# Optimization experiments

Measured on AMD Instinct MI355X. Metric: run time of the kernel, lower is better.

The kernel has to match this reference:

```python
import jax, jax.numpy as jnp
import numpy as np

B, C_IN, C_QKV, N = 8, 12, 36, 4096

def setup_inputs() -> dict:
    key = jax.random.key(0)
    ks = jax.random.split(key, 9)
    s_in = 1.0 / np.sqrt(C_IN)
    s_o = 1.0 / np.sqrt(C_QKV)
    return {
        "x": jax.random.normal(ks[0], (B, C_IN, N), dtype=jnp.float32),
        "wq": jax.random.uniform(ks[1], (C_QKV, C_IN), jnp.float32, -s_in, s_in),
        "bq": jax.random.uniform(ks[2], (C_QKV,), jnp.float32, -s_in, s_in),
        "wk": jax.random.uniform(ks[3], (C_QKV, C_IN), jnp.float32, -s_in, s_in),
        "bk": jax.random.uniform(ks[4], (C_QKV,), jnp.float32, -s_in, s_in),
        "wv": jax.random.uniform(ks[5], (C_QKV, C_IN), jnp.float32, -s_in, s_in),
        "bv": jax.random.uniform(ks[6], (C_QKV,), jnp.float32, -s_in, s_in),
        "wo": jax.random.uniform(ks[7], (C_IN, C_QKV), jnp.float32, -s_o, s_o),
        "bo": jax.random.uniform(ks[8], (C_IN,), jnp.float32, -s_o, s_o),
    }

def _conv1x1(w, b, x):
    # 1x1 Conv1d == channel-mixing matmul: [o,i] @ [b,i,n] -> [b,o,n]
    return jnp.einsum('oi,bin->bon', w, x) + b[None, :, None]

def reference(x, wq, bq, wk, bk, wv, bv, wo, bo):
    scale = 1.0 / jnp.sqrt(jnp.float32(x.shape[1]))  # 1/sqrt(12)
    q = _conv1x1(wq, bq, x)  # [B, 36, N]
    k = _conv1x1(wk, bk, x)
    v = _conv1x1(wv, bv, x)
    # inter = k^T @ q : scores[b,n,m] = sum_c k[b,c,n] * q[b,c,m]
    scores = jnp.einsum('bcn,bcm->bnm', k, q) * scale  # [B, N, N]
    weights = jax.nn.softmax(scores, axis=-1)
    attn = jnp.einsum('bcn,bnm->bcm', v, weights)  # v @ weights, [B, 36, N]
    return _conv1x1(wo, bo, attn)  # [B, 12, N]
```

## Files before the change

### kernel.cpp

```cpp
#include <hip/hip_runtime.h>
#include <hip/hip_bf16.h>
#include <math.h>

#define B 8
#define CIN 12
#define CQ 36
#define CP 48
#define N 4096
#define SCALE 0.28867513459481287f
#define LOG2E 1.4426950408889634f
#define ZSPLIT 8
#define NCHUNK (N / ZSPLIT)
#define NT (NCHUNK / 32)
#define MSPLIT 2

typedef __attribute__((ext_vector_type(4)))  short bf4_t;
typedef __attribute__((ext_vector_type(8)))  short bf8_t;
typedef __attribute__((ext_vector_type(16))) float f32x16;
typedef __attribute__((ext_vector_type(4)))  float f32x4;

__device__ __forceinline__ unsigned short f2bf(float x) {
  unsigned int u = __float_as_uint(x);
  u += 0x7FFFu + ((u >> 16) & 1u);
  return (unsigned short)(u >> 16);
}

#if __has_builtin(__builtin_amdgcn_cvt_pk_bf16_f32)
typedef __attribute__((ext_vector_type(2))) __bf16 bf16x2_t;
__device__ __forceinline__ unsigned pk2bf(float a, float b) {
  bf16x2_t v = __builtin_amdgcn_cvt_pk_bf16_f32(a, b);
  return __builtin_bit_cast(unsigned, v);
}
#else
__device__ __forceinline__ unsigned pk2bf(float a, float b) {
  return (__float_as_uint(a) >> 16) | (__float_as_uint(b) & 0xFFFF0000u);
}
#endif

__device__ __forceinline__ float bf2f(unsigned short u) {
  return __uint_as_float((unsigned)u << 16);
}

__device__ __forceinline__ float exp2fast(float x) {
#if __has_builtin(__builtin_amdgcn_exp2f)
  return __builtin_amdgcn_exp2f(x);
#else
  return exp2f(x);
#endif
}

__device__ __forceinline__ f32x4 mfma16(bf4_t a, bf4_t b, f32x4 c) {
#if __has_builtin(__builtin_amdgcn_mfma_f32_16x16x16bf16_1k)
  return __builtin_amdgcn_mfma_f32_16x16x16bf16_1k(a, b, c, 0, 0, 0);
#else
  bf8_t a8 = {a[0], a[1], a[2], a[3], 0, 0, 0, 0};
  bf8_t b8 = {b[0], b[1], b[2], b[3], 0, 0, 0, 0};
  return __builtin_amdgcn_mfma_f32_16x16x32_bf16(a8, b8, c, 0, 0, 0);
#endif
}

__device__ __forceinline__ bf8_t lds_bf8(const unsigned short* p) {
  uint2 a = *(const uint2*)p;
  uint2 b = *(const uint2*)(p + 4);
  uint4 r{a.x, a.y, b.x, b.y};
  return __builtin_bit_cast(bf8_t, r);
}
__device__ __forceinline__ void wlds16(unsigned short* p, uint4 v) {
  *(uint2*)p = uint2{v.x, v.y};
  *(uint2*)(p + 4) = uint2{v.z, v.w};
}

__global__ __launch_bounds__(256) void qkv_kernel(
    const float* __restrict__ x,
    const float* __restrict__ wq, const float* __restrict__ bq,
    const float* __restrict__ wk, const float* __restrict__ bk,
    const float* __restrict__ wv, const float* __restrict__ bv,
    unsigned short* __restrict__ qT, unsigned short* __restrict__ kT,
    unsigned short* __restrict__ vbf) {
  __shared__ float sw[CQ * CIN];
  __shared__ float sb[CQ];
  int z = blockIdx.y;
  const float* w  = (z == 0) ? wq : (z == 1) ? wk : wv;
  const float* bb = (z == 0) ? bq : (z == 1) ? bk : bv;
  float scale = (z == 1) ? SCALE * LOG2E : 1.0f;
  int tid = threadIdx.x;
  for (int e = tid; e < CQ * CIN; e += 256) sw[e] = w[e] * scale;
  if (tid < CQ) sb[tid] = bb[tid] * scale;
  __syncthreads();
  int gid = blockIdx.x * 256 + tid;
  int b = gid >> 12;
  int n = gid & (N - 1);
  float xv[CIN];
#pragma unroll
  for (int i = 0; i < CIN; ++i) xv[i] = x[(b * CIN + i) * N + n];
  if (z == 2) {
#pragma unroll
    for (int o = 0; o < CQ; ++o) {
      float a = sb[o];
#pragma unroll
      for (int i = 0; i < CIN; ++i) a += sw[o * CIN + i] * xv[i];
      vbf[((size_t)b * CP + o) * N + n] = f2bf(a);
    }
  } else {
    __attribute__((aligned(16))) unsigned row[CP / 2];
#pragma unroll
    for (int o = 0; o < CQ; o += 2) {
      float a0 = sb[o], a1 = sb[o + 1];
#pragma unroll
      for (int i = 0; i < CIN; ++i) {
        float xi = xv[i];
        a0 += sw[o * CIN + i] * xi;
        a1 += sw[(o + 1) * CIN + i] * xi;
      }
      row[o / 2] = (unsigned)f2bf(a0) | ((unsigned)f2bf(a1) << 16);
    }
    row[18] = (z == 0) ? 0x3F803F80u : 0u;
#pragma unroll
    for (int o = 19; o < CP / 2; ++o) row[o] = 0;
    unsigned short* dst = ((z == 0) ? qT : kT) + ((size_t)b * N + n) * CP;
#pragma unroll
    for (int i = 0; i < 6; ++i) *(uint4*)(dst + 8 * i) = *(const uint4*)&row[4 * i];
  }
}

__global__ __launch_bounds__(256) void stats_kernel(
    const unsigned short* __restrict__ qT, const unsigned short* __restrict__ kT,
    float* __restrict__ psum) {
  __shared__ float red[4][64];
  int tid = threadIdx.x, lane = tid & 63, wave = tid >> 6;
  int b = blockIdx.y, nblk = blockIdx.x, ms = blockIdx.z;
  int l31 = lane & 31, h = lane >> 5;
  int n0 = nblk * 64;
  size_t bN = (size_t)b * N;
  const unsigned short* krow0 = kT + (bN + n0 + l31) * CP + h * 8;
  const unsigned short* krow1 = krow0 + (size_t)32 * CP;
  bf8_t a0 = *(const bf8_t*)(krow0);
  bf8_t a1 = *(const bf8_t*)(krow0 + 16);
  bf8_t a2 = *(const bf8_t*)(krow0 + 32);
  bf8_t a3 = *(const bf8_t*)(krow1);
  bf8_t a4 = *(const bf8_t*)(krow1 + 16);
  bf8_t a5 = *(const bf8_t*)(krow1 + 32);
  float rs0[16], rs1[16];
#pragma unroll
  for (int r = 0; r < 16; ++r) { rs0[r] = 0.f; rs1[r] = 0.f; }
  const int MW = N / MSPLIT / 4;
  const unsigned short* qbase =
      qT + (bN + ms * (N / MSPLIT) + wave * MW + l31) * CP + h * 8;
#pragma unroll 2
  for (int t = 0; t < MW / 32; ++t) {
    const unsigned short* qrow2 = qbase + (size_t)t * 32 * CP;
    bf8_t b0 = *(const bf8_t*)(qrow2);
    bf8_t b1 = *(const bf8_t*)(qrow2 + 16);
    bf8_t b2 = *(const bf8_t*)(qrow2 + 32);
    f32x16 S0, S1;
#pragma unroll
    for (int r = 0; r < 16; ++r) { S0[r] = 0.f; S1[r] = 0.f; }
    S0 = __builtin_amdgcn_mfma_f32_32x32x16_bf16(a0, b0, S0, 0, 0, 0);
    S0 = __builtin_amdgcn_mfma_f32_32x32x16_bf16(a1, b1, S0, 0, 0, 0);
    S0 = __builtin_amdgcn_mfma_f32_32x32x16_bf16(a2, b2, S0, 0, 0, 0);
    S1 = __builtin_amdgcn_mfma_f32_32x32x16_bf16(a3, b0, S1, 0, 0, 0);
    S1 = __builtin_amdgcn_mfma_f32_32x32x16_bf16(a4, b1, S1, 0, 0, 0);
    S1 = __builtin_amdgcn_mfma_f32_32x32x16_bf16(a5, b2, S1, 0, 0, 0);
#pragma unroll
    for (int r = 0; r < 16; ++r) {
      rs0[r] += exp2fast(S0[r]);
      rs1[r] += exp2fast(S1[r]);
    }
  }
#pragma unroll
  for (int off = 16; off >= 1; off >>= 1)
#pragma unroll
    for (int r = 0; r < 16; ++r) {
      rs0[r] += __shfl_xor(rs0[r], off, 32);
      rs1[r] += __shfl_xor(rs1[r], off, 32);
    }
  if (l31 == 0) {
#pragma unroll
    for (int r = 0; r < 16; ++r) {
      int row = (r & 3) + 8 * (r >> 2) + 4 * h;
      red[wave][row] = rs0[r];
      red[wave][32 + row] = rs1[r];
    }
  }
  __syncthreads();
  if (tid < 64) {
    float s = red[0][tid] + red[1][tid] + red[2][tid] + red[3][tid];
    psum[((size_t)ms * B + b) * N + n0 + tid] = s;
  }
}

__global__ __launch_bounds__(256) void prep_kernel(
    const float* __restrict__ psum, unsigned short* __restrict__ kT,
    float* __restrict__ out, const float* __restrict__ bo) {
  int bx = blockIdx.x, tid = threadIdx.x;
  if (bx < B * N / 256) {
    int gid = bx * 256 + tid;
    float L = 0.f;
#pragma unroll
    for (int ms = 0; ms < MSPLIT; ++ms) L += psum[(size_t)ms * B * N + gid];
    float t = -__log2f(L);
    unsigned short hi = f2bf(t);
    unsigned short lo = f2bf(t - bf2f(hi));
    size_t base = (size_t)gid * CP;
    kT[base + 36] = hi;
    kT[base + 37] = lo;
  } else {
    int gid = (bx - B * N / 256) * 256 + tid;
    int e4 = gid * 4;
    int i = (e4 >> 12) % CIN;
    float bv = bo[i];
    *(float4*)(out + e4) = float4{bv, bv, bv, bv};
  }
}

__global__ __launch_bounds__(256, 3) void attn_kernel(
    const unsigned short* __restrict__ qT, const unsigned short* __restrict__ kT,
    const unsigned short* __restrict__ vbf, const float* __restrict__ wo,
    float* __restrict__ out) {
  __shared__ unsigned short kbuf[2][32 * 52];
  __shared__ unsigned short vbuf[2][48 * 36];
  __shared__ unsigned short plds[4][2][32 * 40];
  int tid = threadIdx.x, lane = tid & 63, wave = tid >> 6;
  int b = blockIdx.y, z = blockIdx.z, mblk = blockIdx.x;
  int l31 = lane & 31, h = lane >> 5, l15 = lane & 15, q4 = lane >> 4;
  int m0 = mblk * 256 + wave * 64;
  size_t bN = (size_t)b * N;
  bool isK0 = tid < 192;
  int r0row = isK0 ? (tid / 6) : ((tid - 192) >> 2);
  int r0c   = isK0 ? (tid % 6) : ((tid - 192) & 3);
  const unsigned short* s0 = isK0
      ? kT + (bN + z * NCHUNK + r0row) * CP + r0c * 8
      : vbf + ((size_t)b * CP + r0row) * N + z * NCHUNK + r0c * 8;
  int s0stride = isK0 ? 32 * CP : 32;
  unsigned short* dst0 = isK0 ? &kbuf[0][r0row * 52 + r0c * 8]
                              : &vbuf[0][r0row * 36 + r0c * 8];
  int dbs0 = isK0 ? 32 * 52 : 48 * 36;
  bool has1 = tid < 128;
  int r1row = (tid >> 2) + 16;
  int r1c = tid & 3;
  const unsigned short* s1 =
      vbf + ((size_t)b * CP + r1row) * N + z * NCHUNK + r1c * 8;
  unsigned short* dst1 = &vbuf[0][r1row * 36 + r1c * 8];
  const int dbs1 = 48 * 36;
  bf8_t qb[2][3];
#pragma unroll
  for (int mt = 0; mt < 2; ++mt) {
    const unsigned short* qrow = qT + (bN + m0 + mt * 32 + l31) * CP + h * 8;
    qb[mt][0] = *(const bf8_t*)(qrow);
    qb[mt][1] = *(const bf8_t*)(qrow + 16);
    qb[mt][2] = *(const bf8_t*)(qrow + 32);
  }
  bf4_t woa[3];
#pragma unroll
  for (int ct = 0; ct < 3; ++ct) {
    float4 w4 = {0.f, 0.f, 0.f, 0.f};
    int col = 16 * ct + q4 * 4;
    if (l15 < CIN && col < CQ) w4 = *(const float4*)(wo + l15 * CQ + col);
    woa[ct] = bf4_t{(short)f2bf(w4.x), (short)f2bf(w4.y),
                    (short)f2bf(w4.z), (short)f2bf(w4.w)};
  }
  f32x4 acc[2][3][2];
#pragma unroll
  for (int mt = 0; mt < 2; ++mt)
#pragma unroll
    for (int ct = 0; ct < 3; ++ct)
#pragma unroll
      for (int hm = 0; hm < 2; ++hm)
#pragma unroll
        for (int r = 0; r < 4; ++r) acc[mt][ct][hm][r] = 0.f;
  uint4 r0 = *(const uint4*)s0; s0 += s0stride;
  uint4 r1{0, 0, 0, 0};
  if (has1) { r1 = *(const uint4*)s1; s1 += 32; }
  wlds16(dst0, r0);
  if (has1) wlds16(dst1, r1);
  __syncthreads();
  for (int t = 0; t < NT; ++t) {
    int buf = t & 1;
    if (t + 1 < NT) {
      r0 = *(const uint4*)s0; s0 += s0stride;
      if (has1) { r1 = *(const uint4*)s1; s1 += 32; }
    }
    const unsigned short* kb = kbuf[buf];
    const unsigned short* vb = vbuf[buf];
    bf8_t a0 = lds_bf8(kb + l31 * 52 + h * 8);
    bf8_t a1 = lds_bf8(kb + l31 * 52 + h * 8 + 16);
    bf8_t a2 = lds_bf8(kb + l31 * 52 + h * 8 + 32);
#pragma unroll
    for (int mt = 0; mt < 2; ++mt) {
      f32x16 S;
#pragma unroll
      for (int r = 0; r < 16; ++r) S[r] = 0.f;
      S = __builtin_amdgcn_mfma_f32_32x32x16_bf16(a0, qb[mt][0], S, 0, 0, 0);
      S = __builtin_amdgcn_mfma_f32_32x32x16_bf16(a1, qb[mt][1], S, 0, 0, 0);
      S = __builtin_amdgcn_mfma_f32_32x32x16_bf16(a2, qb[mt][2], S, 0, 0, 0);
      unsigned short* pl = plds[wave][mt];
#pragma unroll
      for (int qd = 0; qd < 4; ++qd) {
        uint2 pk;
        pk.x = pk2bf(exp2fast(S[4 * qd + 0]), exp2fast(S[4 * qd + 1]));
        pk.y = pk2bf(exp2fast(S[4 * qd + 2]), exp2fast(S[4 * qd + 3]));
        *(uint2*)&pl[l31 * 40 + 8 * qd + 4 * h] = pk;
      }
    }
    bf8_t v0 = lds_bf8(vb + (0 * 16 + l15) * 36 + q4 * 8);
    bf8_t v1 = lds_bf8(vb + (1 * 16 + l15) * 36 + q4 * 8);
    bf8_t v2 = lds_bf8(vb + (2 * 16 + l15) * 36 + q4 * 8);
#pragma unroll
    for (int mt = 0; mt < 2; ++mt) {
      const unsigned short* pl = plds[wave][mt];
      bf8_t pb0 = *(const bf8_t*)&pl[l15 * 40 + q4 * 8];
      bf8_t pb1 = *(const bf8_t*)&pl[(16 + l15) * 40 + q4 * 8];
      acc[mt][0][0] = __builtin_amdgcn_mfma_f32_16x16x32_bf16(v0, pb0, acc[mt][0][0], 0, 0, 0);
      acc[mt][0][1] = __builtin_amdgcn_mfma_f32_16x16x32_bf16(v0, pb1, acc[mt][0][1], 0, 0, 0);
      acc[mt][1][0] = __builtin_amdgcn_mfma_f32_16x16x32_bf16(v1, pb0, acc[mt][1][0], 0, 0, 0);
      acc[mt][1][1] = __builtin_amdgcn_mfma_f32_16x16x32_bf16(v1, pb1, acc[mt][1][1], 0, 0, 0);
      acc[mt][2][0] = __builtin_amdgcn_mfma_f32_16x16x32_bf16(v2, pb0, acc[mt][2][0], 0, 0, 0);
      acc[mt][2][1] = __builtin_amdgcn_mfma_f32_16x16x32_bf16(v2, pb1, acc[mt][2][1], 0, 0, 0);
    }
    if (t + 1 < NT) {
      int nb = buf ^ 1;
      wlds16(dst0 + nb * dbs0, r0);
      if (has1) wlds16(dst1 + nb * dbs1, r1);
    }
    __syncthreads();
  }
#pragma unroll
  for (int mt = 0; mt < 2; ++mt)
#pragma unroll
    for (int hm = 0; hm < 2; ++hm) {
      f32x4 po = {0.f, 0.f, 0.f, 0.f};
#pragma unroll
      for (int ct = 0; ct < 3; ++ct) {
        union { uint2 u; bf4_t v; } pb;
        pb.u.x = pk2bf(acc[mt][ct][hm][0], acc[mt][ct][hm][1]);
        pb.u.y = pk2bf(acc[mt][ct][hm][2], acc[mt][ct][hm][3]);
        po = mfma16(woa[ct], pb.v, po);
      }
      if (q4 < 3) {
        float* ob = out + ((size_t)b * CIN + q4 * 4) * N + m0 + mt * 32 + hm * 16 + l15;
#pragma unroll
        for (int r = 0; r < 4; ++r) atomicAdd(ob + (size_t)r * N, po[r]);
      }
    }
}

extern "C" void kernel_launch(void* const* d_in, const int* in_sizes, int n_in,
                              void* d_out, int out_size, void* d_ws, size_t ws_size,
                              hipStream_t stream) {
  const float* x  = (const float*)d_in[0];
  const float* wq = (const float*)d_in[1];
  const float* bq = (const float*)d_in[2];
  const float* wk = (const float*)d_in[3];
  const float* bk = (const float*)d_in[4];
  const float* wv = (const float*)d_in[5];
  const float* bv = (const float*)d_in[6];
  const float* wo = (const float*)d_in[7];
  const float* bo = (const float*)d_in[8];
  float* out = (float*)d_out;

  char* ws = (char*)d_ws;
  unsigned short* qT  = (unsigned short*)ws;
  unsigned short* kT  = (unsigned short*)(ws + 3145728);
  unsigned short* vbf = (unsigned short*)(ws + 2 * 3145728);
  float* psum = (float*)(ws + 3 * 3145728);

  qkv_kernel<<<dim3(B * N / 256, 3), 256, 0, stream>>>(x, wq, bq, wk, bk, wv, bv,
                                                       qT, kT, vbf);
  stats_kernel<<<dim3(N / 64, B, MSPLIT), 256, 0, stream>>>(qT, kT, psum);
  prep_kernel<<<B * N / 256 + B * CIN * N / 1024, 256, 0, stream>>>(psum, kT, out, bo);
  attn_kernel<<<dim3(N / 256, B, ZSPLIT), 256, 0, stream>>>(qT, kT, vbf, wo, out);
}
```

Baseline: 135.9 us.

## Fuse four pipeline kernels into one cooperative mega-kernel with grid syncs

Merges the qkv, stats, prep and attention kernels into a single cooperative launch of 1024 blocks, separated by grid-wide barriers, to remove kernel-launch gaps and tail effects between the stages. The qkv stage is also reorganized so that 8 threads share each position and each computes a slice of Q, K or V. In the attention loop the P write/read is interleaved per m-tile, and the LDS buffers are shared through one raw shared array. The change risks grid.sync overhead, and the mega-kernel uses max-size register and LDS limits across all phases, which may lower occupancy. If the cooperative launch fails, it falls back to four per-phase launches.

Result: slower. 515.5 us (+279.4%).

```diff
diff --git a/kernel.cpp b/kernel.cpp
--- a/kernel.cpp
+++ b/kernel.cpp
@@ -1,6 +1,9 @@
 #include <hip/hip_runtime.h>
 #include <hip/hip_bf16.h>
+#include <hip/hip_cooperative_groups.h>
 #include <math.h>
+
+namespace cg = cooperative_groups;
 
 #define B 8
 #define CIN 12
@@ -70,278 +73,293 @@
   *(uint2*)(p + 4) = uint2{v.z, v.w};
 }
 
-__global__ __launch_bounds__(256) void qkv_kernel(
+__global__ __launch_bounds__(256, 4) void mega_kernel(
     const float* __restrict__ x,
     const float* __restrict__ wq, const float* __restrict__ bq,
     const float* __restrict__ wk, const float* __restrict__ bk,
     const float* __restrict__ wv, const float* __restrict__ bv,
+    const float* __restrict__ wo, const float* __restrict__ bo,
     unsigned short* __restrict__ qT, unsigned short* __restrict__ kT,
-    unsigned short* __restrict__ vbf) {
-  __shared__ float sw[CQ * CIN];
-  __shared__ float sb[CQ];
-  int z = blockIdx.y;
-  const float* w  = (z == 0) ? wq : (z == 1) ? wk : wv;
-  const float* bb = (z == 0) ? bq : (z == 1) ? bk : bv;
-  float scale = (z == 1) ? SCALE * LOG2E : 1.0f;
+    unsigned short* __restrict__ vbf, float* __restrict__ psum,
+    float* __restrict__ out, int phase) {
+  __shared__ __align__(16) char smraw[34048];
+  cg::grid_group grid = cg::this_grid();
   int tid = threadIdx.x;
-  for (int e = tid; e < CQ * CIN; e += 256) sw[e] = w[e] * scale;
-  if (tid < CQ) sb[tid] = bb[tid] * scale;
-  __syncthreads();
-  int gid = blockIdx.x * 256 + tid;
-  int b = gid >> 12;
-  int n = gid & (N - 1);
-  float xv[CIN];
-#pragma unroll
-  for (int i = 0; i < CIN; ++i) xv[i] = x[(b * CIN + i) * N + n];
-  if (z == 2) {
-#pragma unroll
-    for (int o = 0; o < CQ; ++o) {
-      float a = sb[o];
-#pragma unroll
-      for (int i = 0; i < CIN; ++i) a += sw[o * CIN + i] * xv[i];
-      vbf[((size_t)b * CP + o) * N + n] = f2bf(a);
-    }
-  } else {
-    __attribute__((aligned(16))) unsigned row[CP / 2];
-#pragma unroll
-    for (int o = 0; o < CQ; o += 2) {
-      float a0 = sb[o], a1 = sb[o + 1];
-#pragma unroll
-      for (int i = 0; i < CIN; ++i) {
-        float xi = xv[i];
-        a0 += sw[o * CIN + i] * xi;
-        a1 += sw[(o + 1) * CIN + i] * xi;
-      }
-      row[o / 2] = (unsigned)f2bf(a0) | ((unsigned)f2bf(a1) << 16);
-    }
-    row[18] = (z == 0) ? 0x3F803F80u : 0u;
-#pragma unroll
-    for (int o = 19; o < CP / 2; ++o) row[o] = 0;
-    unsigned short* dst = ((z == 0) ? qT : kT) + ((size_t)b * N + n) * CP;
-#pragma unroll
-    for (int i = 0; i < 6; ++i) *(uint4*)(dst + 8 * i) = *(const uint4*)&row[4 * i];
-  }
-}
-
-__global__ __launch_bounds__(256) void stats_kernel(
-    const unsigned short* __restrict__ qT, const unsigned short* __restrict__ kT,
-    float* __restrict__ psum) {
-  __shared__ float red[4][64];
-  int tid = threadIdx.x, lane = tid & 63, wave = tid >> 6;
-  int b = blockIdx.y, nblk = blockIdx.x, ms = blockIdx.z;
-  int l31 = lane & 31, h = lane >> 5;
-  int n0 = nblk * 64;
-  size_t bN = (size_t)b * N;
-  const unsigned short* krow0 = kT + (bN + n0 + l31) * CP + h * 8;
-  const unsigned short* krow1 = krow0 + (size_t)32 * CP;
-  bf8_t a0 = *(const bf8_t*)(krow0);
-  bf8_t a1 = *(const bf8_t*)(krow0 + 16);
-  bf8_t a2 = *(const bf8_t*)(krow0 + 32);
-  bf8_t a3 = *(const bf8_t*)(krow1);
-  bf8_t a4 = *(const bf8_t*)(krow1 + 16);
-  bf8_t a5 = *(const bf8_t*)(krow1 + 32);
-  float rs0[16], rs1[16];
-#pragma unroll
-  for (int r = 0; r < 16; ++r) { rs0[r] = 0.f; rs1[r] = 0.f; }
-  const int MW = N / MSPLIT / 4;
-  const unsigned short* qbase =
-      qT + (bN + ms * (N / MSPLIT) + wave * MW + l31) * CP + h * 8;
+  int bx = blockIdx.x;
+
+  if (phase == -1 || phase == 0) {
+    float* sw = (float*)smraw;
+    for (int e = tid; e < CQ * CIN; e += 256) {
+      sw[e] = wq[e];
+      sw[432 + e] = wk[e] * (SCALE * LOG2E);
+      sw[864 + e] = wv[e];
+    }
+    if (tid < CQ) {
+      sw[1296 + tid] = bq[tid];
+      sw[1332 + tid] = bk[tid] * (SCALE * LOG2E);
+      sw[1368 + tid] = bv[tid];
+    }
+    __syncthreads();
+    int p = bx * 32 + (tid >> 3);
+    int slot = tid & 7;
+    int b = p >> 12, n = p & (N - 1);
+    float xv[CIN];
+#pragma unroll
+    for (int i = 0; i < CIN; ++i) xv[i] = x[(b * CIN + i) * N + n];
+    if (slot < 6) {
+      int isK = slot >= 3 ? 1 : 0;
+      int s = slot - 3 * isK;
+      const float* w = sw + 432 * isK;
+      const float* bb2 = sw + 1296 + 36 * isK;
+      unsigned rowu[8];
+#pragma unroll
+      for (int jj = 0; jj < 8; ++jj) {
+        float a2[2];
+#pragma unroll
+        for (int e = 0; e < 2; ++e) {
+          int o = 16 * s + 2 * jj + e;
+          float a;
+          if (o < CQ) {
+            a = bb2[o];
+#pragma unroll
+            for (int i = 0; i < CIN; ++i) a += w[o * CIN + i] * xv[i];
+          } else if (o < 38 && !isK) {
+            a = 1.0f;
+          } else {
+            a = 0.f;
+          }
+          a2[e] = a;
+        }
+        rowu[jj] = pk2bf(a2[0], a2[1]);
+      }
+      unsigned short* dst = (isK ? kT : qT) + ((size_t)b * N + n) * CP + 16 * s;
+      uint4 u0{rowu[0], rowu[1], rowu[2], rowu[3]};
+      uint4 u1{rowu[4], rowu[5], rowu[6], rowu[7]};
+      *(uint4*)dst = u0;
+      *(uint4*)(dst + 8) = u1;
+    } else {
+      int s = slot - 6;
+#pragma unroll
+      for (int j = 0; j < 18; ++j) {
+        int o = 18 * s + j;
+        float a = sw[1368 + o];
+#pragma unroll
+        for (int i = 0; i < CIN; ++i) a += sw[864 + o * CIN + i] * xv[i];
+        vbf[((size_t)b * CP + o) * N + n] = f2bf(a);
+      }
+    }
+  }
+  if (phase == -1) grid.sync();
+
+  if (phase == -1 || phase == 1) {
+    float (*red)[64] = (float(*)[64])smraw;
+    int lane = tid & 63, wave = tid >> 6;
+    int nblk = bx & 63, b = (bx >> 6) & 7, ms = bx >> 9;
+    int l31 = lane & 31, h = lane >> 5;
+    int n0 = nblk * 64;
+    size_t bN = (size_t)b * N;
+    const unsigned short* krow0 = kT + (bN + n0 + l31) * CP + h * 8;
+    const unsigned short* krow1 = krow0 + (size_t)32 * CP;
+    bf8_t a0 = *(const bf8_t*)(krow0);
+    bf8_t a1 = *(const bf8_t*)(krow0 + 16);
+    bf8_t a2 = *(const bf8_t*)(krow0 + 32);
+    bf8_t a3 = *(const bf8_t*)(krow1);
+    bf8_t a4 = *(const bf8_t*)(krow1 + 16);
+    bf8_t a5 = *(const bf8_t*)(krow1 + 32);
+    float rs0[16], rs1[16];
+#pragma unroll
+    for (int r = 0; r < 16; ++r) { rs0[r] = 0.f; rs1[r] = 0.f; }
+    const int MW = N / MSPLIT / 4;
+    const unsigned short* qbase =
+        qT + (bN + ms * (N / MSPLIT) + wave * MW + l31) * CP + h * 8;
 #pragma unroll 2
-  for (int t = 0; t < MW / 32; ++t) {
-    const unsigned short* qrow2 = qbase + (size_t)t * 32 * CP;
-    bf8_t b0 = *(const bf8_t*)(qrow2);
-    bf8_t b1 = *(const bf8_t*)(qrow2 + 16);
-    bf8_t b2 = *(const bf8_t*)(qrow2 + 32);
-    f32x16 S0, S1;
-#pragma unroll
-    for (int r = 0; r < 16; ++r) { S0[r] = 0.f; S1[r] = 0.f; }
-    S0 = __builtin_amdgcn_mfma_f32_32x32x16_bf16(a0, b0, S0, 0, 0, 0);
-    S0 = __builtin_amdgcn_mfma_f32_32x32x16_bf16(a1, b1, S0, 0, 0, 0);
-    S0 = __builtin_amdgcn_mfma_f32_32x32x16_bf16(a2, b2, S0, 0, 0, 0);
-    S1 = __builtin_amdgcn_mfma_f32_32x32x16_bf16(a3, b0, S1, 0, 0, 0);
-    S1 = __builtin_amdgcn_mfma_f32_32x32x16_bf16(a4, b1, S1, 0, 0, 0);
-    S1 = __builtin_amdgcn_mfma_f32_32x32x16_bf16(a5, b2, S1, 0, 0, 0);
-#pragma unroll
-    for (int r = 0; r < 16; ++r) {
-      rs0[r] += exp2fast(S0[r]);
-      rs1[r] += exp2fast(S1[r]);
-    }
-  }
-#pragma unroll
-  for (int off = 16; off >= 1; off >>= 1)
-#pragma unroll
-    for (int r = 0; r < 16; ++r) {
-      rs0[r] += __shfl_xor(rs0[r], off, 32);
-      rs1[r] += __shfl_xor(rs1[r], off, 32);
-    }
-  if (l31 == 0) {
-#pragma unroll
-    for (int r = 0; r < 16; ++r) {
-      int row = (r & 3) + 8 * (r >> 2) + 4 * h;
-      red[wave][row] = rs0[r];
-      red[wave][32 + row] = rs1[r];
-    }
-  }
-  __syncthreads();
-  if (tid < 64) {
-    float s = red[0][tid] + red[1][tid] + red[2][tid] + red[3][tid];
-    psum[((size_t)ms * B + b) * N + n0 + tid] = s;
-  }
-}
-
-__global__ __launch_bounds__(256) void prep_kernel(
-    const float* __restrict__ psum, unsigned short* __restrict__ kT,
-    float* __restrict__ out, const float* __restrict__ bo) {
-  int bx = blockIdx.x, tid = threadIdx.x;
-  if (bx < B * N / 256) {
-    int gid = bx * 256 + tid;
-    float L = 0.f;
-#pragma unroll
-    for (int ms = 0; ms < MSPLIT; ++ms) L += psum[(size_t)ms * B * N + gid];
-    float t = -__log2f(L);
-    unsigned short hi = f2bf(t);
-    unsigned short lo = f2bf(t - bf2f(hi));
-    size_t base = (size_t)gid * CP;
-    kT[base + 36] = hi;
-    kT[base + 37] = lo;
-  } else {
-    int gid = (bx - B * N / 256) * 256 + tid;
-    int e4 = gid * 4;
-    int i = (e4 >> 12) % CIN;
-    float bv = bo[i];
-    *(float4*)(out + e4) = float4{bv, bv, bv, bv};
-  }
-}
-
-__global__ __launch_bounds__(256, 3) void attn_kernel(
-    const unsigned short* __restrict__ qT, const unsigned short* __restrict__ kT,
-    const unsigned short* __restrict__ vbf, const float* __restrict__ wo,
-    float* __restrict__ out) {
-  __shared__ unsigned short kbuf[2][32 * 52];
-  __shared__ unsigned short vbuf[2][48 * 36];
-  __shared__ unsigned short plds[4][2][32 * 40];
-  int tid = threadIdx.x, lane = tid & 63, wave = tid >> 6;
-  int b = blockIdx.y, z = blockIdx.z, mblk = blockIdx.x;
-  int l31 = lane & 31, h = lane >> 5, l15 = lane & 15, q4 = lane >> 4;
-  int m0 = mblk * 256 + wave * 64;
-  size_t bN = (size_t)b * N;
-  bool isK0 = tid < 192;
-  int r0row = isK0 ? (tid / 6) : ((tid - 192) >> 2);
-  int r0c   = isK0 ? (tid % 6) : ((tid - 192) & 3);
-  const unsigned short* s0 = isK0
-      ? kT + (bN + z * NCHUNK + r0row) * CP + r0c * 8
-      : vbf + ((size_t)b * CP + r0row) * N + z * NCHUNK + r0c * 8;
-  int s0stride = isK0 ? 32 * CP : 32;
-  unsigned short* dst0 = isK0 ? &kbuf[0][r0row * 52 + r0c * 8]
-                              : &vbuf[0][r0row * 36 + r0c * 8];
-  int dbs0 = isK0 ? 32 * 52 : 48 * 36;
-  bool has1 = tid < 128;
-  int r1row = (tid >> 2) + 16;
-  int r1c = tid & 3;
-  const unsigned short* s1 =
-      vbf + ((size_t)b * CP + r1row) * N + z * NCHUNK + r1c * 8;
-  unsigned short* dst1 = &vbuf[0][r1row * 36 + r1c * 8];
-  const int dbs1 = 48 * 36;
-  bf8_t qb[2][3];
-#pragma unroll
-  for (int mt = 0; mt < 2; ++mt) {
-    const unsigned short* qrow = qT + (bN + m0 + mt * 32 + l31) * CP + h * 8;
-    qb[mt][0] = *(const bf8_t*)(qrow);
-    qb[mt][1] = *(const bf8_t*)(qrow + 16);
-    qb[mt][2] = *(const bf8_t*)(qrow + 32);
-  }
-  bf4_t woa[3];
-#pragma unroll
-  for (int ct = 0; ct < 3; ++ct) {
-    float4 w4 = {0.f, 0.f, 0.f, 0.f};
-    int col = 16 * ct + q4 * 4;
-    if (l15 < CIN && col < CQ) w4 = *(const float4*)(wo + l15 * CQ + col);
-    woa[ct] = bf4_t{(short)f2bf(w4.x), (short)f2bf(w4.y),
-                    (short)f2bf(w4.z), (short)f2bf(w4.w)};
-  }
-  f32x4 acc[2][3][2];
-#pragma unroll
-  for (int mt = 0; mt < 2; ++mt)
-#pragma unroll
-    for (int ct = 0; ct < 3; ++ct)
-#pragma unroll
-      for (int hm = 0; hm < 2; ++hm)
-#pragma unroll
-        for (int r = 0; r < 4; ++r) acc[mt][ct][hm][r] = 0.f;
-  uint4 r0 = *(const uint4*)s0; s0 += s0stride;
-  uint4 r1{0, 0, 0, 0};
-  if (has1) { r1 = *(const uint4*)s1; s1 += 32; }
-  wlds16(dst0, r0);
-  if (has1) wlds16(dst1, r1);
-  __syncthreads();
-  for (int t = 0; t < NT; ++t) {
-    int buf = t & 1;
-    if (t + 1 < NT) {
-      r0 = *(const uint4*)s0; s0 += s0stride;
-      if (has1) { r1 = *(const uint4*)s1; s1 += 32; }
-    }
-    const unsigned short* kb = kbuf[buf];
-    const unsigned short* vb = vbuf[buf];
-    bf8_t a0 = lds_bf8(kb + l31 * 52 + h * 8);
-    bf8_t a1 = lds_bf8(kb + l31 * 52 + h * 8 + 16);
-    bf8_t a2 = lds_bf8(kb + l31 * 52 + h * 8 + 32);
+    for (int t = 0; t < MW / 32; ++t) {
+      const unsigned short* qrow2 = qbase + (size_t)t * 32 * CP;
+      bf8_t b0 = *(const bf8_t*)(qrow2);
+      bf8_t b1 = *(const bf8_t*)(qrow2 + 16);
+      bf8_t b2 = *(const bf8_t*)(qrow2 + 32);
+      f32x16 S0, S1;
+#pragma unroll
+      for (int r = 0; r < 16; ++r) { S0[r] = 0.f; S1[r] = 0.f; }
+      S0 = __builtin_amdgcn_mfma_f32_32x32x16_bf16(a0, b0, S0, 0, 0, 0);
+      S0 = __builtin_amdgcn_mfma_f32_32x32x16_bf16(a1, b1, S0, 0, 0, 0);
+      S0 = __builtin_amdgcn_mfma_f32_32x32x16_bf16(a2, b2, S0, 0, 0, 0);
+      S1 = __builtin_amdgcn_mfma_f32_32x32x16_bf16(a3, b0, S1, 0, 0, 0);
+      S1 = __builtin_amdgcn_mfma_f32_32x32x16_bf16(a4, b1, S1, 0, 0, 0);
+      S1 = __builtin_amdgcn_mfma_f32_32x32x16_bf16(a5, b2, S1, 0, 0, 0);
+#pragma unroll
+      for (int r = 0; r < 16; ++r) {
+        rs0[r] += exp2fast(S0[r]);
+        rs1[r] += exp2fast(S1[r]);
+      }
+    }
+#pragma unroll
+    for (int off = 16; off >= 1; off >>= 1)
+#pragma unroll
+      for (int r = 0; r < 16; ++r) {
+        rs0[r] += __shfl_xor(rs0[r], off, 32);
+        rs1[r] += __shfl_xor(rs1[r], off, 32);
+      }
+    if (l31 == 0) {
+#pragma unroll
+      for (int r = 0; r < 16; ++r) {
+        int row = (r & 3) + 8 * (r >> 2) + 4 * h;
+        red[wave][row] = rs0[r];
+        red[wave][32 + row] = rs1[r];
+      }
+    }
+    __syncthreads();
+    if (tid < 64) {
+      float s = red[0][tid] + red[1][tid] + red[2][tid] + red[3][tid];
+      psum[((size_t)ms * B + b) * N + n0 + tid] = s;
+    }
+  }
+  if (phase == -1) grid.sync();
+
+  if (phase == -1 || phase == 2) {
+    if (bx < 128) {
+      int gid = bx * 256 + tid;
+      float L = psum[gid] + psum[(size_t)B * N + gid];
+      float t = -__log2f(L);
+      unsigned short hi = f2bf(t);
+      unsigned short lo = f2bf(t - bf2f(hi));
+      size_t base = (size_t)gid * CP;
+      kT[base + 36] = hi;
+      kT[base + 37] = lo;
+    } else if (bx < 512) {
+      int gid = (bx - 128) * 256 + tid;
+      int e4 = gid * 4;
+      int i = (e4 >> 12) % CIN;
+      float bv2 = bo[i];
+      *(float4*)(out + e4) = float4{bv2, bv2, bv2, bv2};
+    }
+  }
+  if (phase == -1) grid.sync();
+
+  if (phase == -1 || phase == 3) {
+    unsigned short* kbuf = (unsigned short*)smraw;
+    unsigned short* vbuf = kbuf + 2 * 32 * 52;
+    unsigned short* plds = vbuf + 2 * 48 * 36;
+    int lane = tid & 63, wave = tid >> 6;
+    int mblk = bx & 15, b = (bx >> 4) & 7, z = bx >> 7;
+    int l31 = lane & 31, h = lane >> 5, l15 = lane & 15, q4 = lane >> 4;
+    int m0 = mblk * 256 + wave * 64;
+    size_t bN = (size_t)b * N;
+    bool isK0 = tid < 192;
+    int r0row = isK0 ? (tid / 6) : ((tid - 192) >> 2);
+    int r0c   = isK0 ? (tid % 6) : ((tid - 192) & 3);
+    const unsigned short* s0 = isK0
+        ? kT + (bN + z * NCHUNK + r0row) * CP + r0c * 8
+        : vbf + ((size_t)b * CP + r0row) * N + z * NCHUNK + r0c * 8;
+    int s0stride = isK0 ? 32 * CP : 32;
+    unsigned short* dst0 = isK0 ? &kbuf[r0row * 52 + r0c * 8]
+                                : &vbuf[r0row * 36 + r0c * 8];
+    int dbs0 = isK0 ? 32 * 52 : 48 * 36;
+    bool has1 = tid < 128;
+    int r1row = (tid >> 2) + 16;
+    int r1c = tid & 3;
+    const unsigned short* s1 =
+        vbf + ((size_t)b * CP + r1row) * N + z * NCHUNK + r1c * 8;
+    unsigned short* dst1 = &vbuf[r1row * 36 + r1c * 8];
+    const int dbs1 = 48 * 36;
+    bf8_t qb[2][3];
 #pragma unroll
     for (int mt = 0; mt < 2; ++mt) {
-      f32x16 S;
-#pragma unroll
-      for (int r = 0; r < 16; ++r) S[r] = 0.f;
-      S = __builtin_amdgcn_mfma_f32_32x32x16_bf16(a0, qb[mt][0], S, 0, 0, 0);
-      S = __builtin_amdgcn_mfma_f32_32x32x16_bf16(a1, qb[mt][1], S, 0, 0, 0);
-      S = __builtin_amdgcn_mfma_f32_32x32x16_bf16(a2, qb[mt][2], S, 0, 0, 0);
-      unsigned short* pl = plds[wave][mt];
-#pragma unroll
-      for (int qd = 0; qd < 4; ++qd) {
-        uint2 pk;
-        pk.x = pk2bf(exp2fast(S[4 * qd + 0]), exp2fast(S[4 * qd + 1]));
-        pk.y = pk2bf(exp2fast(S[4 * qd + 2]), exp2fast(S[4 * qd + 3]));
-        *(uint2*)&pl[l31 * 40 + 8 * qd + 4 * h] = pk;
-      }
-    }
-    bf8_t v0 = lds_bf8(vb + (0 * 16 + l15) * 36 + q4 * 8);
-    bf8_t v1 = lds_bf8(vb + (1 * 16 + l15) * 36 + q4 * 8);
-    bf8_t v2 = lds_bf8(vb + (2 * 16 + l15) * 36 + q4 * 8);
-#pragma unroll
-    for (int mt = 0; mt < 2; ++mt) {
-      const unsigned short* pl = plds[wave][mt];
-      bf8_t pb0 = *(const bf8_t*)&pl[l15 * 40 + q4 * 8];
-      bf8_t pb1 = *(const bf8_t*)&pl[(16 + l15) * 40 + q4 * 8];
-      acc[mt][0][0] = __builtin_amdgcn_mfma_f32_16x16x32_bf16(v0, pb0, acc[mt][0][0], 0, 0, 0);
-      acc[mt][0][1] = __builtin_amdgcn_mfma_f32_16x16x32_bf16(v0, pb1, acc[mt][0][1], 0, 0, 0);
-      acc[mt][1][0] = __builtin_amdgcn_mfma_f32_16x16x32_bf16(v1, pb0, acc[mt][1][0], 0, 0, 0);
-      acc[mt][1][1] = __builtin_amdgcn_mfma_f32_16x16x32_bf16(v1, pb1, acc[mt][1][1], 0, 0, 0);
-      acc[mt][2][0] = __builtin_amdgcn_mfma_f32_16x16x32_bf16(v2, pb0, acc[mt][2][0], 0, 0, 0);
-      acc[mt][2][1] = __builtin_amdgcn_mfma_f32_16x16x32_bf16(v2, pb1, acc[mt][2][1], 0, 0, 0);
-    }
-    if (t + 1 < NT) {
-      int nb = buf ^ 1;
-      wlds16(dst0 + nb * dbs0, r0);
-      if (has1) wlds16(dst1 + nb * dbs1, r1);
-    }
+      const unsigned short* qrow = qT + (bN + m0 + mt * 32 + l31) * CP + h * 8;
+      qb[mt][0] = *(const bf8_t*)(qrow);
+      qb[mt][1] = *(const bf8_t*)(qrow + 16);
+      qb[mt][2] = *(const bf8_t*)(qrow + 32);
+    }
+    bf4_t woa[3];
+#pragma unroll
+    for (int ct = 0; ct < 3; ++ct) {
+      float4 w4 = {0.f, 0.f, 0.f, 0.f};
+      int col = 16 * ct + q4 * 4;
+      if (l15 < CIN && col < CQ) w4 = *(const float4*)(wo + l15 * CQ + col);
+      woa[ct] = bf4_t{(short)f2bf(w4.x), (short)f2bf(w4.y),
+                      (short)f2bf(w4.z), (short)f2bf(w4.w)};
+    }
+    f32x4 acc[2][3][2];
+#pragma unroll
+    for (int mt = 0; mt < 2; ++mt)
+#pragma unroll
+      for (int ct = 0; ct < 3; ++ct)
+#pragma unroll
+        for (int hm = 0; hm < 2; ++hm)
+#pragma unroll
+          for (int r = 0; r < 4; ++r) acc[mt][ct][hm][r] = 0.f;
+    uint4 r0 = *(const uint4*)s0; s0 += s0stride;
+    uint4 r1{0, 0, 0, 0};
+    if (has1) { r1 = *(const uint4*)s1; s1 += 32; }
     __syncthreads();
-  }
-#pragma unroll
-  for (int mt = 0; mt < 2; ++mt)
-#pragma unroll
-    for (int hm = 0; hm < 2; ++hm) {
-      f32x4 po = {0.f, 0.f, 0.f, 0.f};
-#pragma unroll
-      for (int ct = 0; ct < 3; ++ct) {
-        union { uint2 u; bf4_t v; } pb;
-        pb.u.x = pk2bf(acc[mt][ct][hm][0], acc[mt][ct][hm][1]);
-        pb.u.y = pk2bf(acc[mt][ct][hm][2], acc[mt][ct][hm][3]);
-        po = mfma16(woa[ct], pb.v, po);
-      }
-      if (q4 < 3) {
-        float* ob = out + ((size_t)b * CIN + q4 * 4) * N + m0 + mt * 32 + hm * 16 + l15;
-#pragma unroll
-        for (int r = 0; r < 4; ++r) atomicAdd(ob + (size_t)r * N, po[r]);
-      }
-    }
+    wlds16(dst0, r0);
+    if (has1) wlds16(dst1, r1);
+    __syncthreads();
+    for (int t = 0; t < NT; ++t) {
+      int buf = t & 1;
+      if (t + 1 < NT) {
+        r0 = *(const uint4*)s0; s0 += s0stride;
+        if (has1) { r1 = *(const uint4*)s1; s1 += 32; }
+      }
+      const unsigned short* kb = kbuf + buf * (32 * 52);
+      const unsigned short* vb = vbuf + buf * (48 * 36);
+      bf8_t a0 = lds_bf8(kb + l31 * 52 + h * 8);
+      bf8_t a1 = lds_bf8(kb + l31 * 52 + h * 8 + 16);
+      bf8_t a2 = lds_bf8(kb + l31 * 52 + h * 8 + 32);
+      bf8_t v0 = lds_bf8(vb + (0 * 16 + l15) * 36 + q4 * 8);
+      bf8_t v1 = lds_bf8(vb + (1 * 16 + l15) * 36 + q4 * 8);
+      bf8_t v2 = lds_bf8(vb + (2 * 16 + l15) * 36 + q4 * 8);
+#pragma unroll
+      for (int mt = 0; mt < 2; ++mt) {
+        f32x16 S;
+#pragma unroll
+        for (int r = 0; r < 16; ++r) S[r] = 0.f;
+        S = __builtin_amdgcn_mfma_f32_32x32x16_bf16(a0, qb[mt][0], S, 0, 0, 0);
+        S = __builtin_amdgcn_mfma_f32_32x32x16_bf16(a1, qb[mt][1], S, 0, 0, 0);
+        S = __builtin_amdgcn_mfma_f32_32x32x16_bf16(a2, qb[mt][2], S, 0, 0, 0);
+        unsigned short* pl = plds + (wave * 2 + mt) * (32 * 40);
+#pragma unroll
+        for (int qd = 0; qd < 4; ++qd) {
+          uint2 pk;
+          pk.x = pk2bf(exp2fast(S[4 * qd + 0]), exp2fast(S[4 * qd + 1]));
+          pk.y = pk2bf(exp2fast(S[4 * qd + 2]), exp2fast(S[4 * qd + 3]));
+          *(uint2*)&pl[l31 * 40 + 8 * qd + 4 * h] = pk;
+        }
+        bf8_t pb0 = *(const bf8_t*)&pl[l15 * 40 + q4 * 8];
+        bf8_t pb1 = *(const bf8_t*)&pl[(16 + l15) * 40 + q4 * 8];
+        acc[mt][0][0] = __builtin_amdgcn_mfma_f32_16x16x32_bf16(v0, pb0, acc[mt][0][0], 0, 0, 0);
+        acc[mt][0][1] = __builtin_amdgcn_mfma_f32_16x16x32_bf16(v0, pb1, acc[mt][0][1], 0, 0, 0);
+        acc[mt][1][0] = __builtin_amdgcn_mfma_f32_16x16x32_bf16(v1, pb0, acc[mt][1][0], 0, 0, 0);
+        acc[mt][1][1] = __builtin_amdgcn_mfma_f32_16x16x32_bf16(v1, pb1, acc[mt][1][1], 0, 0, 0);
+        acc[mt][2][0] = __builtin_amdgcn_mfma_f32_16x16x32_bf16(v2, pb0, acc[mt][2][0], 0, 0, 0);
+        acc[mt][2][1] = __builtin_amdgcn_mfma_f32_16x16x32_bf16(v2, pb1, acc[mt][2][1], 0, 0, 0);
+      }
+      if (t + 1 < NT) {
+        int nb = buf ^ 1;
+        wlds16(dst0 + nb * dbs0, r0);
+        if (has1) wlds16(dst1 + nb * dbs1, r1);
+      }
+      __syncthreads();
+    }
+#pragma unroll
+    for (int mt = 0; mt < 2; ++mt)
+#pragma unroll
+      for (int hm = 0; hm < 2; ++hm) {
+        f32x4 po = {0.f, 0.f, 0.f, 0.f};
+#pragma unroll
+        for (int ct = 0; ct < 3; ++ct) {
+          union { uint2 u; bf4_t v; } pb;
+          pb.u.x = pk2bf(acc[mt][ct][hm][0], acc[mt][ct][hm][1]);
+          pb.u.y = pk2bf(acc[mt][ct][hm][2], acc[mt][ct][hm][3]);
+          po = mfma16(woa[ct], pb.v, po);
+        }
+        if (q4 < 3) {
+          float* ob = out + ((size_t)b * CIN + q4 * 4) * N + m0 + mt * 32 + hm * 16 + l15;
+#pragma unroll
+          for (int r = 0; r < 4; ++r) atomicAdd(ob + (size_t)r * N, po[r]);
+        }
+      }
+  }
 }
 
 extern "C" void kernel_launch(void* const* d_in, const int* in_sizes, int n_in,
@@ -364,9 +382,16 @@
   unsigned short* vbf = (unsigned short*)(ws + 2 * 3145728);
   float* psum = (float*)(ws + 3 * 3145728);
 
-  qkv_kernel<<<dim3(B * N / 256, 3), 256, 0, stream>>>(x, wq, bq, wk, bk, wv, bv,
-                                                       qT, kT, vbf);
-  stats_kernel<<<dim3(N / 64, B, MSPLIT), 256, 0, stream>>>(qT, kT, psum);
-  prep_kernel<<<B * N / 256 + B * CIN * N / 1024, 256, 0, stream>>>(psum, kT, out, bo);
-  attn_kernel<<<dim3(N / 256, B, ZSPLIT), 256, 0, stream>>>(qT, kT, vbf, wo, out);
-}
+  int phaseAll = -1;
+  void* args[] = {(void*)&x,  (void*)&wq, (void*)&bq, (void*)&wk, (void*)&bk,
+                  (void*)&wv, (void*)&bv, (void*)&wo, (void*)&bo,
+                  (void*)&qT, (void*)&kT, (void*)&vbf, (void*)&psum,
+                  (void*)&out, (void*)&phaseAll};
+  hipError_t err = hipLaunchCooperativeKernel(
+      (const void*)mega_kernel, dim3(1024), dim3(256), args, 0, stream);
+  if (err != hipSuccess) {
+    for (int ph = 0; ph < 4; ++ph)
+      mega_kernel<<<dim3(1024), dim3(256), 0, stream>>>(
+          x, wq, bq, wk, bk, wv, bv, wo, bo, qT, kT, vbf, psum, out, ph);
+  }
+}
```

## Fold prep kernel into qkv and stats kernels using last-block atomic counter

Applied to the files above, without the earlier changes.

Removes the separate prep launch. Output bias initialisation and counter reset now run as extra blocks of the qkv kernel. The final log-sum normalisation is done inside the stats kernel by whichever of the two m-split blocks finishes last, detected with a threadfence and an atomic counter. In the attention loop the V fragment loads are hoisted before the score MFMAs and the two mt loops are merged. This saves one kernel launch and a pass over psum, at the cost of atomics and fences in the stats kernel.

Result: slower. 213.8 us (+57.3%).

```diff
diff --git a/kernel.cpp b/kernel.cpp
--- a/kernel.cpp
+++ b/kernel.cpp
@@ -75,25 +75,36 @@
     const float* __restrict__ wq, const float* __restrict__ bq,
     const float* __restrict__ wk, const float* __restrict__ bk,
     const float* __restrict__ wv, const float* __restrict__ bv,
+    const float* __restrict__ bo,
     unsigned short* __restrict__ qT, unsigned short* __restrict__ kT,
-    unsigned short* __restrict__ vbf) {
+    unsigned short* __restrict__ vbf, float* __restrict__ out,
+    int* __restrict__ cnt) {
   __shared__ float sw[CQ * CIN];
   __shared__ float sb[CQ];
-  int z = blockIdx.y;
-  const float* w  = (z == 0) ? wq : (z == 1) ? wk : wv;
-  const float* bb = (z == 0) ? bq : (z == 1) ? bk : bv;
-  float scale = (z == 1) ? SCALE * LOG2E : 1.0f;
-  int tid = threadIdx.x;
+  int bx = blockIdx.x, tid = threadIdx.x;
+  int role = bx >> 7; if (role > 3) role = 3;
+  if (role == 3) {
+    if (bx == 384) { cnt[tid] = 0; cnt[256 + tid] = 0; }
+    int gid = (bx - 384) * 256 + tid;
+    int e4 = gid * 4;
+    int i = (e4 >> 12) % CIN;
+    float bv2 = bo[i];
+    *(float4*)(out + e4) = float4{bv2, bv2, bv2, bv2};
+    return;
+  }
+  const float* w  = (role == 0) ? wq : (role == 1) ? wk : wv;
+  const float* bb = (role == 0) ? bq : (role == 1) ? bk : bv;
+  float scale = (role == 1) ? SCALE * LOG2E : 1.0f;
   for (int e = tid; e < CQ * CIN; e += 256) sw[e] = w[e] * scale;
   if (tid < CQ) sb[tid] = bb[tid] * scale;
   __syncthreads();
-  int gid = blockIdx.x * 256 + tid;
+  int gid = (bx & 127) * 256 + tid;
   int b = gid >> 12;
   int n = gid & (N - 1);
   float xv[CIN];
 #pragma unroll
   for (int i = 0; i < CIN; ++i) xv[i] = x[(b * CIN + i) * N + n];
-  if (z == 2) {
+  if (role == 2) {
 #pragma unroll
     for (int o = 0; o < CQ; ++o) {
       float a = sb[o];
@@ -114,21 +125,22 @@
       }
       row[o / 2] = (unsigned)f2bf(a0) | ((unsigned)f2bf(a1) << 16);
     }
-    row[18] = (z == 0) ? 0x3F803F80u : 0u;
+    row[18] = (role == 0) ? 0x3F803F80u : 0u;
 #pragma unroll
     for (int o = 19; o < CP / 2; ++o) row[o] = 0;
-    unsigned short* dst = ((z == 0) ? qT : kT) + ((size_t)b * N + n) * CP;
+    unsigned short* dst = ((role == 0) ? qT : kT) + ((size_t)b * N + n) * CP;
 #pragma unroll
     for (int i = 0; i < 6; ++i) *(uint4*)(dst + 8 * i) = *(const uint4*)&row[4 * i];
   }
 }
 
 __global__ __launch_bounds__(256) void stats_kernel(
-    const unsigned short* __restrict__ qT, const unsigned short* __restrict__ kT,
-    float* __restrict__ psum) {
+    const unsigned short* __restrict__ qT, unsigned short* __restrict__ kT,
+    float* __restrict__ psum, int* __restrict__ cnt) {
   __shared__ float red[4][64];
+  __shared__ int lastflag;
   int tid = threadIdx.x, lane = tid & 63, wave = tid >> 6;
-  int b = blockIdx.y, nblk = blockIdx.x, ms = blockIdx.z;
+  int nblk = blockIdx.x, b = blockIdx.y, ms = blockIdx.z;
   int l31 = lane & 31, h = lane >> 5;
   int n0 = nblk * 64;
   size_t bN = (size_t)b * N;
@@ -187,29 +199,23 @@
     float s = red[0][tid] + red[1][tid] + red[2][tid] + red[3][tid];
     psum[((size_t)ms * B + b) * N + n0 + tid] = s;
   }
-}
-
-__global__ __launch_bounds__(256) void prep_kernel(
-    const float* __restrict__ psum, unsigned short* __restrict__ kT,
-    float* __restrict__ out, const float* __restrict__ bo) {
-  int bx = blockIdx.x, tid = threadIdx.x;
-  if (bx < B * N / 256) {
-    int gid = bx * 256 + tid;
-    float L = 0.f;
-#pragma unroll
-    for (int ms = 0; ms < MSPLIT; ++ms) L += psum[(size_t)ms * B * N + gid];
+  __threadfence();
+  __syncthreads();
+  if (tid == 0) {
+    int old = atomicAdd(&cnt[b * 64 + nblk], 1);
+    lastflag = (old == MSPLIT - 1);
+  }
+  __syncthreads();
+  if (lastflag && tid < 64) {
+    __threadfence();
+    float L = psum[(size_t)b * N + n0 + tid] +
+              psum[(size_t)(B + b) * N + n0 + tid];
     float t = -__log2f(L);
     unsigned short hi = f2bf(t);
     unsigned short lo = f2bf(t - bf2f(hi));
-    size_t base = (size_t)gid * CP;
+    size_t base = (bN + n0 + tid) * CP;
     kT[base + 36] = hi;
     kT[base + 37] = lo;
-  } else {
-    int gid = (bx - B * N / 256) * 256 + tid;
-    int e4 = gid * 4;
-    int i = (e4 >> 12) % CIN;
-    float bv = bo[i];
-    *(float4*)(out + e4) = float4{bv, bv, bv, bv};
   }
 }
 
@@ -221,7 +227,7 @@
   __shared__ unsigned short vbuf[2][48 * 36];
   __shared__ unsigned short plds[4][2][32 * 40];
   int tid = threadIdx.x, lane = tid & 63, wave = tid >> 6;
-  int b = blockIdx.y, z = blockIdx.z, mblk = blockIdx.x;
+  int mblk = blockIdx.x, b = blockIdx.y, z = blockIdx.z;
   int l31 = lane & 31, h = lane >> 5, l15 = lane & 15, q4 = lane >> 4;
   int m0 = mblk * 256 + wave * 64;
   size_t bN = (size_t)b * N;
@@ -285,6 +291,9 @@
     bf8_t a0 = lds_bf8(kb + l31 * 52 + h * 8);
     bf8_t a1 = lds_bf8(kb + l31 * 52 + h * 8 + 16);
     bf8_t a2 = lds_bf8(kb + l31 * 52 + h * 8 + 32);
+    bf8_t v0 = lds_bf8(vb + (0 * 16 + l15) * 36 + q4 * 8);
+    bf8_t v1 = lds_bf8(vb + (1 * 16 + l15) * 36 + q4 * 8);
+    bf8_t v2 = lds_bf8(vb + (2 * 16 + l15) * 36 + q4 * 8);
 #pragma unroll
     for (int mt = 0; mt < 2; ++mt) {
       f32x16 S;
@@ -301,13 +310,6 @@
         pk.y = pk2bf(exp2fast(S[4 * qd + 2]), exp2fast(S[4 * qd + 3]));
         *(uint2*)&pl[l31 * 40 + 8 * qd + 4 * h] = pk;
       }
-    }
-    bf8_t v0 = lds_bf8(vb + (0 * 16 + l15) * 36 + q4 * 8);
-    bf8_t v1 = lds_bf8(vb + (1 * 16 + l15) * 36 + q4 * 8);
-    bf8_t v2 = lds_bf8(vb + (2 * 16 + l15) * 36 + q4 * 8);
-#pragma unroll
-    for (int mt = 0; mt < 2; ++mt) {
-      const unsigned short* pl = plds[wave][mt];
       bf8_t pb0 = *(const bf8_t*)&pl[l15 * 40 + q4 * 8];
       bf8_t pb1 = *(const bf8_t*)&pl[(16 + l15) * 40 + q4 * 8];
       acc[mt][0][0] = __builtin_amdgcn_mfma_f32_16x16x32_bf16(v0, pb0, acc[mt][0][0], 0, 0, 0);
@@ -363,10 +365,10 @@
   unsigned short* kT  = (unsigned short*)(ws + 3145728);
   unsigned short* vbf = (unsigned short*)(ws + 2 * 3145728);
   float* psum = (float*)(ws + 3 * 3145728);
-
-  qkv_kernel<<<dim3(B * N / 256, 3), 256, 0, stream>>>(x, wq, bq, wk, bk, wv, bv,
-                                                       qT, kT, vbf);
-  stats_kernel<<<dim3(N / 64, B, MSPLIT), 256, 0, stream>>>(qT, kT, psum);
-  prep_kernel<<<B * N / 256 + B * CIN * N / 1024, 256, 0, stream>>>(psum, kT, out, bo);
+  int* cnt    = (int*)(ws + 3 * 3145728 + 262144);
+
+  qkv_kernel<<<dim3(768), 256, 0, stream>>>(x, wq, bq, wk, bk, wv, bv, bo,
+                                            qT, kT, vbf, out, cnt);
+  stats_kernel<<<dim3(N / 64, B, MSPLIT), 256, 0, stream>>>(qT, kT, psum, cnt);
   attn_kernel<<<dim3(N / 256, B, ZSPLIT), 256, 0, stream>>>(qT, kT, vbf, wo, out);
 }
```
